# Kernel optimization log

Hardware: AMD Instinct MI355X
Metric: run time of the kernel (lower is better)

## Reference

```python
import jax, jax.numpy as jnp
import numpy as np
import math

B, T, D, H, FF = 2, 2048, 1024, 16, 4096
DH = D // H
EPS = 1e-5

def _ternary(key, out_f, in_f):
    # TFLELayer: ternary-quantized linear weight in {-1,0,1} (stored as f32 here)
    return jax.random.randint(key, (out_f, in_f), -1, 2).astype(jnp.float32)

def setup_inputs() -> dict:
    key = jax.random.key(0)
    ks = jax.random.split(key, 8)
    x = jax.random.normal(ks[0], (B, T, D), dtype=jnp.float32)
    mask = jnp.triu(jnp.ones((T, T), dtype=bool), k=1)  # True = masked (causal)
    return {
        "x": x,
        "mask": mask,
        "ln1_g": jnp.ones((D,), jnp.float32), "ln1_b": jnp.zeros((D,), jnp.float32),
        "ln2_g": jnp.ones((D,), jnp.float32), "ln2_b": jnp.zeros((D,), jnp.float32),
        "Wq": _ternary(ks[1], D, D), "Wk": _ternary(ks[2], D, D),
        "Wv": _ternary(ks[3], D, D), "Wo": _ternary(ks[4], D, D),
        "Wff1": _ternary(ks[5], FF, D), "Wff2": _ternary(ks[6], D, FF),
    }

def _ln(x, g, b):
    mu = jnp.mean(x, axis=-1, keepdims=True)
    var = jnp.var(x, axis=-1, keepdims=True)
    return (x - mu) * jax.lax.rsqrt(var + EPS) * g + b

def reference(x, mask, ln1_g, ln1_b, ln2_g, ln2_b, Wq, Wk, Wv, Wo, Wff1, Wff2):
    h = _ln(x, ln1_g, ln1_b)
    q = (h @ Wq.T).reshape(B, T, H, DH).transpose(0, 2, 1, 3)  # (B,H,T,DH)
    k = (h @ Wk.T).reshape(B, T, H, DH).transpose(0, 2, 1, 3)
    v = (h @ Wv.T).reshape(B, T, H, DH).transpose(0, 2, 1, 3)
    scale = 1.0 / math.sqrt(DH)
    attn = jnp.einsum('bhqd,bhkd->bhqk', q, k) * scale
    attn = jnp.where(mask[None, None], -jnp.inf, attn)
    attn = jax.nn.softmax(attn, axis=-1)
    out = jnp.einsum('bhqk,bhkd->bhqd', attn, v)
    out = out.transpose(0, 2, 1, 3).reshape(B, T, D) @ Wo.T
    x = x + out
    h = _ln(x, ln2_g, ln2_b)
    ff = jax.nn.gelu(h @ Wff1.T, approximate=False)
    ff = ff @ Wff2.T
    return x + ff
```

## Files before the change

kernel.cpp:

```cpp
#include <hip/hip_runtime.h>

typedef __bf16 bf16;
typedef bf16 bf16x8 __attribute__((ext_vector_type(8)));
typedef bf16 bf16x4 __attribute__((ext_vector_type(4)));
typedef float f32x4 __attribute__((ext_vector_type(4)));

static __device__ __forceinline__ void async16(const void* g, void* l) {
  __builtin_amdgcn_global_load_lds((__attribute__((address_space(1))) void*)g,
                                   (__attribute__((address_space(3))) void*)l,
                                   16, 0, 0);
}

template <int N>
static __device__ __forceinline__ float ror16(float x) {
  const int y =
      __builtin_amdgcn_update_dpp(0, __float_as_int(x), 0x120 | N, 0xf, 0xf, true);
  return __int_as_float(y);
}
static __device__ __forceinline__ float rowmax16(float x) {
  x = fmaxf(x, ror16<8>(x));
  x = fmaxf(x, ror16<4>(x));
  x = fmaxf(x, ror16<2>(x));
  x = fmaxf(x, ror16<1>(x));
  return x;
}
static __device__ __forceinline__ float rowsum16(float x) {
  x += ror16<8>(x);
  x += ror16<4>(x);
  x += ror16<2>(x);
  x += ror16<1>(x);
  return x;
}

__global__ __launch_bounds__(256) void cvt4(const float* __restrict__ a,
                                            const float* __restrict__ b,
                                            const float* __restrict__ c,
                                            const float* __restrict__ d,
                                            bf16* __restrict__ dst) {
  const size_t i = ((size_t)blockIdx.x * 256 + threadIdx.x) * 4;
  const size_t M1 = 1u << 20;
  const float* src = (i < M1) ? a : (i < 2 * M1) ? b : (i < 3 * M1) ? c : d;
  const size_t off = i & (M1 - 1);
  const float4 v = *(const float4*)(src + off);
  bf16x4 o = {(bf16)v.x, (bf16)v.y, (bf16)v.z, (bf16)v.w};
  *(bf16x4*)(dst + i) = o;
}

__global__ __launch_bounds__(256) void cvt2(const float* __restrict__ a,
                                            const float* __restrict__ b,
                                            bf16* __restrict__ dst) {
  const size_t i = ((size_t)blockIdx.x * 256 + threadIdx.x) * 4;
  const size_t M4 = 4u << 20;
  const float* src = (i < M4) ? a : b;
  const size_t off = (i < M4) ? i : i - M4;
  const float4 v = *(const float4*)(src + off);
  bf16x4 o = {(bf16)v.x, (bf16)v.y, (bf16)v.z, (bf16)v.w};
  *(bf16x4*)(dst + i) = o;
}

template <int EPI, bool SPLIT>
static __device__ __forceinline__ void gemm_body(
    const bf16* __restrict__ A, const bf16* __restrict__ A2,
    const bf16* __restrict__ B, void* __restrict__ Cv, void* __restrict__ C2,
    const float* __restrict__ R, float scale, int col0, int row0, int M, int N,
    int K) {
  __shared__ bf16 sA[128 * 32];
  __shared__ bf16 sB[128 * 32];
  const int tid = threadIdx.x;
  const int lane = tid & 63;
  const int wid = tid >> 6;
  const int wm = wid >> 1, wn = wid & 1;

  f32x4 acc[4][4];
  const f32x4 fzero = {0.f, 0.f, 0.f, 0.f};
#pragma unroll
  for (int i = 0; i < 4; ++i)
#pragma unroll
    for (int j = 0; j < 4; ++j) acc[i][j] = fzero;

  const int nk = K >> 5;
  const int total = SPLIT ? (nk << 1) : nk;
  const int r0 = tid >> 2, c0 = (tid & 3) << 3;
  const int r1 = (256 + tid) >> 2, c1 = ((256 + tid) & 3) << 3;
  bf16* lA0 = sA + (wid << 6) * 8;
  bf16* lA1 = sA + (256 + (wid << 6)) * 8;
  bf16* lB0 = sB + (wid << 6) * 8;
  bf16* lB1 = sB + (256 + (wid << 6)) * 8;

  for (int kt = 0; kt < total; ++kt) {
    const int kk = (kt < nk) ? kt : kt - nk;
    const bf16* Ap = (SPLIT && kt >= nk) ? A2 : A;
    const int k0 = kk << 5;
    async16(Ap + (size_t)(row0 + r0) * K + k0 + c0, lA0);
    async16(Ap + (size_t)(row0 + r1) * K + k0 + c1, lA1);
    async16(B + (size_t)(col0 + r0) * K + k0 + c0, lB0);
    async16(B + (size_t)(col0 + r1) * K + k0 + c1, lB1);
    __syncthreads();
    const int fr = lane & 15, fq = (lane >> 4) << 3;
    bf16x8 af[4], bfr[4];
#pragma unroll
    for (int i = 0; i < 4; ++i)
      af[i] = *(const bf16x8*)&sA[(wm * 64 + i * 16 + fr) * 32 + fq];
#pragma unroll
    for (int j = 0; j < 4; ++j)
      bfr[j] = *(const bf16x8*)&sB[(wn * 64 + j * 16 + fr) * 32 + fq];
#pragma unroll
    for (int i = 0; i < 4; ++i)
#pragma unroll
      for (int j = 0; j < 4; ++j)
        acc[i][j] = __builtin_amdgcn_mfma_f32_16x16x32_bf16(af[i], bfr[j],
                                                            acc[i][j], 0, 0, 0);
    __syncthreads();
  }

  const int fr = lane & 15, fq4 = (lane >> 4) << 2;
#pragma unroll
  for (int i = 0; i < 4; ++i) {
#pragma unroll
    for (int j = 0; j < 4; ++j) {
      const int rbase = row0 + wm * 64 + i * 16 + fq4;
      const int col = col0 + wn * 64 + j * 16 + fr;
      if constexpr (EPI == 5) {
        const int b = rbase >> 11, t = rbase & 2047;
        const int hh = col >> 6, d = col & 63;
        bf16x4 o4 = {(bf16)acc[i][j][0], (bf16)acc[i][j][1],
                     (bf16)acc[i][j][2], (bf16)acc[i][j][3]};
        *(bf16x4*)&((bf16*)Cv)[(((size_t)(b * 16 + hh)) * 64 + d) * 2048 + t] =
            o4;
      } else {
#pragma unroll
        for (int r = 0; r < 4; ++r) {
          const size_t idx = (size_t)(rbase + r) * N + col;
          const float val = acc[i][j][r];
          if constexpr (EPI == 0) {
            ((float*)Cv)[idx] = val;
          } else if constexpr (EPI == 2) {
            ((float*)Cv)[idx] = val + R[idx];
          } else if constexpr (EPI == 3) {
            ((bf16*)Cv)[idx] =
                (bf16)(0.5f * val * (1.0f + erff(val * 0.7071067811865476f)));
          } else {
            const float vs = val * scale;
            const bf16 hi = (bf16)vs;
            ((bf16*)Cv)[idx] = hi;
            ((bf16*)C2)[idx] = (bf16)(vs - (float)hi);
          }
        }
      }
    }
  }
}

template <int EPI, bool SPLIT>
__global__ __launch_bounds__(256) void gemm_bt(
    const bf16* __restrict__ A, const bf16* __restrict__ A2,
    const bf16* __restrict__ B, void* __restrict__ Cv,
    const float* __restrict__ R, int M, int N, int K) {
  gemm_body<EPI, SPLIT>(A, A2, B, Cv, nullptr, R, 1.0f, blockIdx.x * 128,
                        blockIdx.y * 128, M, N, K);
}

static __device__ __forceinline__ void gemm_split_merged(
    const bf16* __restrict__ A, const bf16* __restrict__ A2,
    const bf16* __restrict__ B, bf16* __restrict__ Chi, bf16* __restrict__ Clo,
    float scale, int col0, int row0) {
  constexpr int K = 1024, N = 1024;
  __shared__ bf16 sAh[128 * 32];
  __shared__ bf16 sAl[128 * 32];
  __shared__ bf16 sB[128 * 32];
  const int tid = threadIdx.x;
  const int lane = tid & 63;
  const int wid = tid >> 6;
  const int wm = wid >> 1, wn = wid & 1;

  f32x4 acc[4][4];
  const f32x4 fzero = {0.f, 0.f, 0.f, 0.f};
#pragma unroll
  for (int i = 0; i < 4; ++i)
#pragma unroll
    for (int j = 0; j < 4; ++j) acc[i][j] = fzero;

  const int r0 = tid >> 2, c0 = (tid & 3) << 3;
  const int r1 = (256 + tid) >> 2, c1 = ((256 + tid) & 3) << 3;
  bf16* lAh0 = sAh + (wid << 6) * 8;
  bf16* lAh1 = sAh + (256 + (wid << 6)) * 8;
  bf16* lAl0 = sAl + (wid << 6) * 8;
  bf16* lAl1 = sAl + (256 + (wid << 6)) * 8;
  bf16* lB0 = sB + (wid << 6) * 8;
  bf16* lB1 = sB + (256 + (wid << 6)) * 8;

  for (int kt = 0; kt < 32; ++kt) {
    const int k0 = kt << 5;
    async16(A + (size_t)(row0 + r0) * K + k0 + c0, lAh0);
    async16(A + (size_t)(row0 + r1) * K + k0 + c1, lAh1);
    async16(A2 + (size_t)(row0 + r0) * K + k0 + c0, lAl0);
    async16(A2 + (size_t)(row0 + r1) * K + k0 + c1, lAl1);
    async16(B + (size_t)(col0 + r0) * K + k0 + c0, lB0);
    async16(B + (size_t)(col0 + r1) * K + k0 + c1, lB1);
    __syncthreads();
    const int fr = lane & 15, fq = (lane >> 4) << 3;
    bf16x8 ah[4], al[4], bfr[4];
#pragma unroll
    for (int i = 0; i < 4; ++i) {
      ah[i] = *(const bf16x8*)&sAh[(wm * 64 + i * 16 + fr) * 32 + fq];
      al[i] = *(const bf16x8*)&sAl[(wm * 64 + i * 16 + fr) * 32 + fq];
    }
#pragma unroll
    for (int j = 0; j < 4; ++j)
      bfr[j] = *(const bf16x8*)&sB[(wn * 64 + j * 16 + fr) * 32 + fq];
#pragma unroll
    for (int i = 0; i < 4; ++i)
#pragma unroll
      for (int j = 0; j < 4; ++j) {
        acc[i][j] = __builtin_amdgcn_mfma_f32_16x16x32_bf16(ah[i], bfr[j],
                                                            acc[i][j], 0, 0, 0);
        acc[i][j] = __builtin_amdgcn_mfma_f32_16x16x32_bf16(al[i], bfr[j],
                                                            acc[i][j], 0, 0, 0);
      }
    __syncthreads();
  }

  const int fr = lane & 15, fq4 = (lane >> 4) << 2;
#pragma unroll
  for (int i = 0; i < 4; ++i)
#pragma unroll
    for (int j = 0; j < 4; ++j) {
      const int rbase = row0 + wm * 64 + i * 16 + fq4;
      const int col = col0 + wn * 64 + j * 16 + fr;
#pragma unroll
      for (int r = 0; r < 4; ++r) {
        const size_t idx = (size_t)(rbase + r) * N + col;
        const float vs = acc[i][j][r] * scale;
        const bf16 hi = (bf16)vs;
        Chi[idx] = hi;
        Clo[idx] = (bf16)(vs - (float)hi);
      }
    }
}

__global__ __launch_bounds__(256) void gemm_qkv(
    const bf16* __restrict__ A, const bf16* __restrict__ A2,
    const bf16* __restrict__ Bq, const bf16* __restrict__ Bk,
    const bf16* __restrict__ Bv, bf16* qh, bf16* ql, bf16* kh, bf16* kl,
    bf16* vt) {
  const int which = blockIdx.x >> 3;
  const int col0 = (blockIdx.x & 7) * 128, row0 = blockIdx.y * 128;
  if (which == 2) {
    gemm_body<5, false>(A, nullptr, Bv, (void*)vt, nullptr, nullptr, 1.0f,
                        col0, row0, 4096, 1024, 1024);
  } else {
    gemm_split_merged(A, A2, which ? Bk : Bq, which ? kh : qh, which ? kl : ql,
                      which ? 1.0f : 0.125f, col0, row0);
  }
}

template <int EPI>
__global__ __launch_bounds__(256) void gemm_bt64(
    const bf16* __restrict__ A, const bf16* __restrict__ B,
    void* __restrict__ Cv, const float* __restrict__ R, int M, int N, int K) {
  __shared__ bf16 sA[128 * 32];
  __shared__ bf16 sB[64 * 32];
  const int col0 = blockIdx.x * 64, row0 = blockIdx.y * 128;
  const int tid = threadIdx.x;
  const int lane = tid & 63;
  const int wid = tid >> 6;
  const int wm = wid >> 1, wn = wid & 1;

  f32x4 acc[4][2];
  const f32x4 fzero = {0.f, 0.f, 0.f, 0.f};
#pragma unroll
  for (int i = 0; i < 4; ++i)
#pragma unroll
    for (int j = 0; j < 2; ++j) acc[i][j] = fzero;

  const int nk = K >> 5;
  const int r0 = tid >> 2, c0 = (tid & 3) << 3;
  const int r1 = (256 + tid) >> 2, c1 = ((256 + tid) & 3) << 3;
  bf16* lA0 = sA + (wid << 6) * 8;
  bf16* lA1 = sA + (256 + (wid << 6)) * 8;
  bf16* lB0 = sB + (wid << 6) * 8;

  for (int kt = 0; kt < nk; ++kt) {
    const int k0 = kt << 5;
    async16(A + (size_t)(row0 + r0) * K + k0 + c0, lA0);
    async16(A + (size_t)(row0 + r1) * K + k0 + c1, lA1);
    async16(B + (size_t)(col0 + r0) * K + k0 + c0, lB0);
    __syncthreads();
    const int fr = lane & 15, fq = (lane >> 4) << 3;
    bf16x8 af[4], bfr[2];
#pragma unroll
    for (int i = 0; i < 4; ++i)
      af[i] = *(const bf16x8*)&sA[(wm * 64 + i * 16 + fr) * 32 + fq];
#pragma unroll
    for (int j = 0; j < 2; ++j)
      bfr[j] = *(const bf16x8*)&sB[(wn * 32 + j * 16 + fr) * 32 + fq];
#pragma unroll
    for (int i = 0; i < 4; ++i)
#pragma unroll
      for (int j = 0; j < 2; ++j)
        acc[i][j] = __builtin_amdgcn_mfma_f32_16x16x32_bf16(af[i], bfr[j],
                                                            acc[i][j], 0, 0, 0);
    __syncthreads();
  }

  const int fr = lane & 15, fq4 = (lane >> 4) << 2;
#pragma unroll
  for (int i = 0; i < 4; ++i) {
#pragma unroll
    for (int j = 0; j < 2; ++j) {
      const int rbase = row0 + wm * 64 + i * 16 + fq4;
      const int col = col0 + wn * 32 + j * 16 + fr;
#pragma unroll
      for (int r = 0; r < 4; ++r) {
        const size_t idx = (size_t)(rbase + r) * N + col;
        const float val = acc[i][j][r];
        if constexpr (EPI == 2) {
          ((float*)Cv)[idx] = val + R[idx];
        } else {
          ((float*)Cv)[idx] = val;
        }
      }
    }
  }
}

template <bool SPLIT>
__global__ __launch_bounds__(256) void ln_kernel(
    const float* __restrict__ x, const float* __restrict__ g,
    const float* __restrict__ b, bf16* __restrict__ hi, bf16* __restrict__ lo) {
  const int row = blockIdx.x;
  const int tid = threadIdx.x;
  const float* xr = x + (size_t)row * 1024;
  float v[4];
  float s1 = 0.f, s2 = 0.f;
#pragma unroll
  for (int j = 0; j < 4; ++j) {
    v[j] = xr[j * 256 + tid];
    s1 += v[j];
    s2 += v[j] * v[j];
  }
#pragma unroll
  for (int off = 1; off < 64; off <<= 1) {
    s1 += __shfl_xor(s1, off);
    s2 += __shfl_xor(s2, off);
  }
  __shared__ float ws1[4], ws2[4];
  const int wid = tid >> 6;
  if ((tid & 63) == 0) {
    ws1[wid] = s1;
    ws2[wid] = s2;
  }
  __syncthreads();
  s1 = ws1[0] + ws1[1] + ws1[2] + ws1[3];
  s2 = ws2[0] + ws2[1] + ws2[2] + ws2[3];
  const float mu = s1 * (1.f / 1024.f);
  const float var = s2 * (1.f / 1024.f) - mu * mu;
  const float rstd = 1.0f / sqrtf(var + 1e-5f);
#pragma unroll
  for (int j = 0; j < 4; ++j) {
    const int cc = j * 256 + tid;
    const float y = (v[j] - mu) * rstd * g[cc] + b[cc];
    const bf16 yh = (bf16)y;
    hi[(size_t)row * 1024 + cc] = yh;
    if constexpr (SPLIT) lo[(size_t)row * 1024 + cc] = (bf16)(y - (float)yh);
  }
}

__global__ __launch_bounds__(256) void attn_kernel(
    const bf16* __restrict__ qh_g, const bf16* __restrict__ ql_g,
    const bf16* __restrict__ kh_g, const bf16* __restrict__ kl_g,
    const bf16* __restrict__ vt_g, bf16* __restrict__ out) {
  __shared__ bf16 lds[18688];
  bf16* Kh = lds;
  bf16* Kl = lds + 4608;
  bf16* Vt = lds + 9216;
  bf16* Ps = lds + 13824;

  const int bid = blockIdx.x;
  const int qt = 31 - (bid >> 5);
  const int h = bid & 15;
  const int b = (bid >> 4) & 1;
  const int t0 = qt << 6;
  const int tid = threadIdx.x;
  const int w = tid >> 6;
  const int lane = tid & 63;
  const int c = lane & 15;
  const int quad = lane >> 4;

  const int r0 = tid >> 3, c0 = (tid & 7) << 3;
  const int r1 = (tid + 256) >> 3, c1 = ((tid + 256) & 7) << 3;

  const size_t qrow =
      ((size_t)(b * 2048 + t0 + w * 16 + c)) * 1024 + h * 64 + quad * 8;
  bf16x8 aqh[2], aql[2];
  aqh[0] = *(const bf16x8*)&qh_g[qrow];
  aqh[1] = *(const bf16x8*)&qh_g[qrow + 32];
  aql[0] = *(const bf16x8*)&ql_g[qrow];
  aql[1] = *(const bf16x8*)&ql_g[qrow + 32];

  f32x4 o[4];
  const f32x4 fzero = {0.f, 0.f, 0.f, 0.f};
#pragma unroll
  for (int j = 0; j < 4; ++j) o[j] = fzero;
  float m_i[4] = {-3e38f, -3e38f, -3e38f, -3e38f};
  float l_i[4] = {0.f, 0.f, 0.f, 0.f};

  const size_t vtb = ((size_t)(b * 16 + h)) * 64 * 2048;
  const size_t kband = ((size_t)(b * 2048)) * 1024 + h * 64;

  bf16x8 gk[6];
  {
    gk[0] = *(const bf16x8*)&kh_g[kband + (size_t)r0 * 1024 + c0];
    gk[1] = *(const bf16x8*)&kh_g[kband + (size_t)r1 * 1024 + c1];
    gk[2] = *(const bf16x8*)&kl_g[kband + (size_t)r0 * 1024 + c0];
    gk[3] = *(const bf16x8*)&kl_g[kband + (size_t)r1 * 1024 + c1];
    gk[4] = *(const bf16x8*)&vt_g[vtb + (size_t)r0 * 2048 + c0];
    gk[5] = *(const bf16x8*)&vt_g[vtb + (size_t)r1 * 2048 + c1];
  }

  for (int kt = 0; kt <= qt; ++kt) {
    __syncthreads();
    *(bf16x8*)&Kh[r0 * 72 + c0] = gk[0];
    *(bf16x8*)&Kh[r1 * 72 + c1] = gk[1];
    *(bf16x8*)&Kl[r0 * 72 + c0] = gk[2];
    *(bf16x8*)&Kl[r1 * 72 + c1] = gk[3];
    *(bf16x8*)&Vt[r0 * 72 + c0] = gk[4];
    *(bf16x8*)&Vt[r1 * 72 + c1] = gk[5];
    __syncthreads();

    if (kt < qt) {
      const int kb1 = (kt + 1) << 6;
      const size_t kbase = kband + (size_t)kb1 * 1024;
      gk[0] = *(const bf16x8*)&kh_g[kbase + (size_t)r0 * 1024 + c0];
      gk[1] = *(const bf16x8*)&kh_g[kbase + (size_t)r1 * 1024 + c1];
      gk[2] = *(const bf16x8*)&kl_g[kbase + (size_t)r0 * 1024 + c0];
      gk[3] = *(const bf16x8*)&kl_g[kbase + (size_t)r1 * 1024 + c1];
      gk[4] = *(const bf16x8*)&vt_g[vtb + (size_t)r0 * 2048 + kb1 + c0];
      gk[5] = *(const bf16x8*)&vt_g[vtb + (size_t)r1 * 2048 + kb1 + c1];
    }

    bf16x8 bkh[4][2], bkl[4][2];
#pragma unroll
    for (int j = 0; j < 4; ++j)
#pragma unroll
      for (int s = 0; s < 2; ++s) {
        bkh[j][s] = *(const bf16x8*)&Kh[(j * 16 + c) * 72 + s * 32 + quad * 8];
        bkl[j][s] = *(const bf16x8*)&Kl[(j * 16 + c) * 72 + s * 32 + quad * 8];
      }

    f32x4 s4[4];
#pragma unroll
    for (int j = 0; j < 4; ++j) s4[j] = fzero;
#pragma unroll
    for (int j = 0; j < 4; ++j)
#pragma unroll
      for (int s = 0; s < 2; ++s) {
        s4[j] = __builtin_amdgcn_mfma_f32_16x16x32_bf16(aqh[s], bkh[j][s], s4[j], 0, 0, 0);
        s4[j] = __builtin_amdgcn_mfma_f32_16x16x32_bf16(aqh[s], bkl[j][s], s4[j], 0, 0, 0);
        s4[j] = __builtin_amdgcn_mfma_f32_16x16x32_bf16(aql[s], bkh[j][s], s4[j], 0, 0, 0);
      }

    if (kt == qt) {
#pragma unroll
      for (int j = 0; j < 4; ++j)
#pragma unroll
        for (int r = 0; r < 4; ++r)
          if (j * 16 + c > w * 16 + quad * 4 + r) s4[j][r] = -3e38f;
    }

    float al[4], p[4][4];
#pragma unroll
    for (int r = 0; r < 4; ++r) {
      float mt = fmaxf(fmaxf(s4[0][r], s4[1][r]), fmaxf(s4[2][r], s4[3][r]));
      mt = rowmax16(mt);
      const float mn = fmaxf(m_i[r], mt);
      al[r] = __expf(m_i[r] - mn);
      float ps = 0.f;
#pragma unroll
      for (int j = 0; j < 4; ++j) {
        p[r][j] = __expf(s4[j][r] - mn);
        ps += p[r][j];
      }
      ps = rowsum16(ps);
      l_i[r] = l_i[r] * al[r] + ps;
      m_i[r] = mn;
#pragma unroll
      for (int j = 0; j < 4; ++j) o[j][r] *= al[r];
    }

    bf16* Pw = Ps + w * 16 * 76;
#pragma unroll
    for (int r = 0; r < 4; ++r)
#pragma unroll
      for (int j = 0; j < 4; ++j)
        Pw[(quad * 4 + r) * 76 + j * 16 + c] = (bf16)p[r][j];

    bf16x8 ap[2], bv[4][2];
#pragma unroll
    for (int s = 0; s < 2; ++s)
      ap[s] = *(const bf16x8*)&Pw[c * 76 + s * 32 + quad * 8];
#pragma unroll
    for (int j = 0; j < 4; ++j)
#pragma unroll
      for (int s = 0; s < 2; ++s)
        bv[j][s] = *(const bf16x8*)&Vt[(j * 16 + c) * 72 + s * 32 + quad * 8];
#pragma unroll
    for (int j = 0; j < 4; ++j)
#pragma unroll
      for (int s = 0; s < 2; ++s)
        o[j] = __builtin_amdgcn_mfma_f32_16x16x32_bf16(ap[s], bv[j][s], o[j], 0, 0, 0);
  }

#pragma unroll
  for (int r = 0; r < 4; ++r) {
    const float inv = 1.0f / l_i[r];
#pragma unroll
    for (int j = 0; j < 4; ++j) {
      const size_t oi =
          ((size_t)(b * 2048 + t0 + w * 16 + quad * 4 + r)) * 1024 + h * 64 +
          j * 16 + c;
      out[oi] = (bf16)(o[j][r] * inv);
    }
  }
}

extern "C" void kernel_launch(void* const* d_in, const int* in_sizes, int n_in,
                              void* d_out, int out_size, void* d_ws,
                              size_t ws_size, hipStream_t stream) {
  const float* x = (const float*)d_in[0];
  const float* g1 = (const float*)d_in[2];
  const float* b1 = (const float*)d_in[3];
  const float* g2 = (const float*)d_in[4];
  const float* b2 = (const float*)d_in[5];
  const float* Wq = (const float*)d_in[6];
  const float* Wk = (const float*)d_in[7];
  const float* Wv = (const float*)d_in[8];
  const float* Wo = (const float*)d_in[9];
  const float* Wf1 = (const float*)d_in[10];
  const float* Wf2 = (const float*)d_in[11];
  char* ws = (char*)d_ws;
  const size_t MB = 1024 * 1024;
  const size_t M1 = 1u << 20;
  bf16* Wq_b = (bf16*)ws;
  bf16* Wk_b = Wq_b + 1 * M1;
  bf16* Wv_b = Wq_b + 2 * M1;
  bf16* Wo_b = Wq_b + 3 * M1;
  bf16* h_hi = (bf16*)(ws + 8 * MB);
  bf16* h_lo = (bf16*)(ws + 16 * MB);
  bf16* Wf1_b = h_hi;
  bf16* Wf2_b = h_lo;
  bf16* qh = (bf16*)(ws + 24 * MB);
  bf16* ql = (bf16*)(ws + 32 * MB);
  bf16* kh = (bf16*)(ws + 40 * MB);
  bf16* kl = (bf16*)(ws + 48 * MB);
  bf16* vt = (bf16*)(ws + 56 * MB);
  bf16* attnout = (bf16*)(ws + 64 * MB);
  float* x1 = (float*)qh;
  bf16* h2 = (bf16*)(ws + 72 * MB);
  bf16* ff = kh;
  float* outp = (float*)d_out;

  cvt4<<<4096, 256, 0, stream>>>(Wq, Wk, Wv, Wo, Wq_b);
  ln_kernel<true><<<4096, 256, 0, stream>>>(x, g1, b1, h_hi, h_lo);
  gemm_qkv<<<dim3(24, 32), 256, 0, stream>>>(h_hi, h_lo, Wq_b, Wk_b, Wv_b, qh,
                                             ql, kh, kl, vt);
  cvt2<<<8192, 256, 0, stream>>>(Wf1, Wf2, Wf1_b);
  attn_kernel<<<1024, 256, 0, stream>>>(qh, ql, kh, kl, vt, attnout);
  gemm_bt64<2><<<dim3(16, 32), 256, 0, stream>>>(attnout, Wo_b, (void*)x1, x,
                                                 4096, 1024, 1024);
  ln_kernel<false><<<4096, 256, 0, stream>>>(x1, g2, b2, h2, nullptr);
  gemm_bt<3, false><<<dim3(32, 32), 256, 0, stream>>>(
      h2, nullptr, Wf1_b, (void*)ff, nullptr, 4096, 4096, 1024);
  gemm_bt64<2><<<dim3(16, 32), 256, 0, stream>>>(ff, Wf2_b, (void*)outp, x1,
                                                 4096, 1024, 4096);
}
```

Baseline: 465.6 us.

## Double attention query tile per block and share LDS across QKV GEMM paths

The attention kernel now handles 128 query rows per block: each wave processes two 16-row sub-tiles against the same K/V tile loaded into LDS. This halves the grid and the repeated K/V global loads per query row. The block order is also changed to interleave long and short causal tiles. Separately, the QKV GEMM paths now take one shared LDS buffer instead of separate static arrays, which lowers that kernel's LDS footprint. The larger attention tile raises register pressure and leaves fewer blocks to balance the causal work.

```diff
diff --git a/kernel.cpp b/kernel.cpp
--- a/kernel.cpp
+++ b/kernel.cpp
@@ -61,11 +61,11 @@
 template <int EPI, bool SPLIT>
 static __device__ __forceinline__ void gemm_body(
     const bf16* __restrict__ A, const bf16* __restrict__ A2,
-    const bf16* __restrict__ B, void* __restrict__ Cv, void* __restrict__ C2,
-    const float* __restrict__ R, float scale, int col0, int row0, int M, int N,
+    const bf16* __restrict__ B, void* __restrict__ Cv,
+    const float* __restrict__ R, bf16* smem, int col0, int row0, int M, int N,
     int K) {
-  __shared__ bf16 sA[128 * 32];
-  __shared__ bf16 sB[128 * 32];
+  bf16* sA = smem;
+  bf16* sB = smem + 4096;
   const int tid = threadIdx.x;
   const int lane = tid & 63;
   const int wid = tid >> 6;
@@ -136,14 +136,9 @@
             ((float*)Cv)[idx] = val;
           } else if constexpr (EPI == 2) {
             ((float*)Cv)[idx] = val + R[idx];
-          } else if constexpr (EPI == 3) {
+          } else {
             ((bf16*)Cv)[idx] =
                 (bf16)(0.5f * val * (1.0f + erff(val * 0.7071067811865476f)));
-          } else {
-            const float vs = val * scale;
-            const bf16 hi = (bf16)vs;
-            ((bf16*)Cv)[idx] = hi;
-            ((bf16*)C2)[idx] = (bf16)(vs - (float)hi);
           }
         }
       }
@@ -156,18 +151,19 @@
     const bf16* __restrict__ A, const bf16* __restrict__ A2,
     const bf16* __restrict__ B, void* __restrict__ Cv,
     const float* __restrict__ R, int M, int N, int K) {
-  gemm_body<EPI, SPLIT>(A, A2, B, Cv, nullptr, R, 1.0f, blockIdx.x * 128,
+  __shared__ bf16 smem[8192];
+  gemm_body<EPI, SPLIT>(A, A2, B, Cv, R, smem, blockIdx.x * 128,
                         blockIdx.y * 128, M, N, K);
 }
 
 static __device__ __forceinline__ void gemm_split_merged(
     const bf16* __restrict__ A, const bf16* __restrict__ A2,
     const bf16* __restrict__ B, bf16* __restrict__ Chi, bf16* __restrict__ Clo,
-    float scale, int col0, int row0) {
+    bf16* smem, float scale, int col0, int row0) {
   constexpr int K = 1024, N = 1024;
-  __shared__ bf16 sAh[128 * 32];
-  __shared__ bf16 sAl[128 * 32];
-  __shared__ bf16 sB[128 * 32];
+  bf16* sAh = smem;
+  bf16* sAl = smem + 4096;
+  bf16* sB = smem + 8192;
   const int tid = threadIdx.x;
   const int lane = tid & 63;
   const int wid = tid >> 6;
@@ -243,14 +239,15 @@
     const bf16* __restrict__ Bq, const bf16* __restrict__ Bk,
     const bf16* __restrict__ Bv, bf16* qh, bf16* ql, bf16* kh, bf16* kl,
     bf16* vt) {
+  __shared__ bf16 smem[12288];
   const int which = blockIdx.x >> 3;
   const int col0 = (blockIdx.x & 7) * 128, row0 = blockIdx.y * 128;
   if (which == 2) {
-    gemm_body<5, false>(A, nullptr, Bv, (void*)vt, nullptr, nullptr, 1.0f,
-                        col0, row0, 4096, 1024, 1024);
+    gemm_body<5, false>(A, nullptr, Bv, (void*)vt, nullptr, smem, col0, row0,
+                        4096, 1024, 1024);
   } else {
     gemm_split_merged(A, A2, which ? Bk : Bq, which ? kh : qh, which ? kl : ql,
-                      which ? 1.0f : 0.125f, col0, row0);
+                      smem, which ? 1.0f : 0.125f, col0, row0);
   }
 }
 
@@ -377,10 +374,11 @@
   bf16* Ps = lds + 13824;
 
   const int bid = blockIdx.x;
-  const int qt = 31 - (bid >> 5);
+  const int g = bid >> 5;
+  const int qt = (g < 8) ? (15 - g) : (g - 8);
   const int h = bid & 15;
   const int b = (bid >> 4) & 1;
-  const int t0 = qt << 6;
+  const int t0 = qt << 7;
   const int tid = threadIdx.x;
   const int w = tid >> 6;
   const int lane = tid & 63;
@@ -390,23 +388,36 @@
   const int r0 = tid >> 3, c0 = (tid & 7) << 3;
   const int r1 = (tid + 256) >> 3, c1 = ((tid + 256) & 7) << 3;
 
-  const size_t qrow =
-      ((size_t)(b * 2048 + t0 + w * 16 + c)) * 1024 + h * 64 + quad * 8;
-  bf16x8 aqh[2], aql[2];
-  aqh[0] = *(const bf16x8*)&qh_g[qrow];
-  aqh[1] = *(const bf16x8*)&qh_g[qrow + 32];
-  aql[0] = *(const bf16x8*)&ql_g[qrow];
-  aql[1] = *(const bf16x8*)&ql_g[qrow + 32];
-
-  f32x4 o[4];
+  bf16x8 aqh[2][2], aql[2][2];
+#pragma unroll
+  for (int u = 0; u < 2; ++u) {
+    const size_t qrow =
+        ((size_t)(b * 2048 + t0 + w * 32 + u * 16 + c)) * 1024 + h * 64 +
+        quad * 8;
+    aqh[u][0] = *(const bf16x8*)&qh_g[qrow];
+    aqh[u][1] = *(const bf16x8*)&qh_g[qrow + 32];
+    aql[u][0] = *(const bf16x8*)&ql_g[qrow];
+    aql[u][1] = *(const bf16x8*)&ql_g[qrow + 32];
+  }
+
+  f32x4 o[2][4];
   const f32x4 fzero = {0.f, 0.f, 0.f, 0.f};
 #pragma unroll
-  for (int j = 0; j < 4; ++j) o[j] = fzero;
-  float m_i[4] = {-3e38f, -3e38f, -3e38f, -3e38f};
-  float l_i[4] = {0.f, 0.f, 0.f, 0.f};
+  for (int u = 0; u < 2; ++u)
+#pragma unroll
+    for (int j = 0; j < 4; ++j) o[u][j] = fzero;
+  float m_i[2][4], l_i[2][4];
+#pragma unroll
+  for (int u = 0; u < 2; ++u)
+#pragma unroll
+    for (int r = 0; r < 4; ++r) {
+      m_i[u][r] = -3e38f;
+      l_i[u][r] = 0.f;
+    }
 
   const size_t vtb = ((size_t)(b * 16 + h)) * 64 * 2048;
   const size_t kband = ((size_t)(b * 2048)) * 1024 + h * 64;
+  const int nt = 2 * qt + 2;
 
   bf16x8 gk[6];
   {
@@ -418,7 +429,8 @@
     gk[5] = *(const bf16x8*)&vt_g[vtb + (size_t)r1 * 2048 + c1];
   }
 
-  for (int kt = 0; kt <= qt; ++kt) {
+  for (int kt = 0; kt < nt; ++kt) {
+    const int kb = kt << 6;
     __syncthreads();
     *(bf16x8*)&Kh[r0 * 72 + c0] = gk[0];
     *(bf16x8*)&Kh[r1 * 72 + c1] = gk[1];
@@ -428,7 +440,7 @@
     *(bf16x8*)&Vt[r1 * 72 + c1] = gk[5];
     __syncthreads();
 
-    if (kt < qt) {
+    if (kt < nt - 1) {
       const int kb1 = (kt + 1) << 6;
       const size_t kbase = kband + (size_t)kb1 * 1024;
       gk[0] = *(const bf16x8*)&kh_g[kbase + (size_t)r0 * 1024 + c0];
@@ -439,89 +451,95 @@
       gk[5] = *(const bf16x8*)&vt_g[vtb + (size_t)r1 * 2048 + kb1 + c1];
     }
 
-    bf16x8 bkh[4][2], bkl[4][2];
+    bf16x8 bkh[4][2], bkl[4][2], bv[4][2];
 #pragma unroll
     for (int j = 0; j < 4; ++j)
 #pragma unroll
       for (int s = 0; s < 2; ++s) {
         bkh[j][s] = *(const bf16x8*)&Kh[(j * 16 + c) * 72 + s * 32 + quad * 8];
         bkl[j][s] = *(const bf16x8*)&Kl[(j * 16 + c) * 72 + s * 32 + quad * 8];
-      }
-
-    f32x4 s4[4];
-#pragma unroll
-    for (int j = 0; j < 4; ++j) s4[j] = fzero;
-#pragma unroll
-    for (int j = 0; j < 4; ++j)
-#pragma unroll
-      for (int s = 0; s < 2; ++s) {
-        s4[j] = __builtin_amdgcn_mfma_f32_16x16x32_bf16(aqh[s], bkh[j][s], s4[j], 0, 0, 0);
-        s4[j] = __builtin_amdgcn_mfma_f32_16x16x32_bf16(aqh[s], bkl[j][s], s4[j], 0, 0, 0);
-        s4[j] = __builtin_amdgcn_mfma_f32_16x16x32_bf16(aql[s], bkh[j][s], s4[j], 0, 0, 0);
-      }
-
-    if (kt == qt) {
+        bv[j][s] = *(const bf16x8*)&Vt[(j * 16 + c) * 72 + s * 32 + quad * 8];
+      }
+
+    bf16* Pw = Ps + w * 16 * 76;
+#pragma unroll
+    for (int u = 0; u < 2; ++u) {
+      f32x4 s4[4];
+#pragma unroll
+      for (int j = 0; j < 4; ++j) s4[j] = fzero;
 #pragma unroll
       for (int j = 0; j < 4; ++j)
 #pragma unroll
-        for (int r = 0; r < 4; ++r)
-          if (j * 16 + c > w * 16 + quad * 4 + r) s4[j][r] = -3e38f;
-    }
-
-    float al[4], p[4][4];
+        for (int s = 0; s < 2; ++s) {
+          s4[j] = __builtin_amdgcn_mfma_f32_16x16x32_bf16(aqh[u][s], bkh[j][s],
+                                                          s4[j], 0, 0, 0);
+          s4[j] = __builtin_amdgcn_mfma_f32_16x16x32_bf16(aqh[u][s], bkl[j][s],
+                                                          s4[j], 0, 0, 0);
+          s4[j] = __builtin_amdgcn_mfma_f32_16x16x32_bf16(aql[u][s], bkh[j][s],
+                                                          s4[j], 0, 0, 0);
+        }
+
+      if (kt >= 2 * qt) {
+        const int qrow0 = t0 + w * 32 + u * 16 + quad * 4;
+#pragma unroll
+        for (int j = 0; j < 4; ++j)
+#pragma unroll
+          for (int r = 0; r < 4; ++r)
+            if (kb + j * 16 + c > qrow0 + r) s4[j][r] = -3e38f;
+      }
+
+      float al[4], p[4][4];
+#pragma unroll
+      for (int r = 0; r < 4; ++r) {
+        float mt = fmaxf(fmaxf(s4[0][r], s4[1][r]), fmaxf(s4[2][r], s4[3][r]));
+        mt = rowmax16(mt);
+        const float mn = fmaxf(m_i[u][r], mt);
+        al[r] = __expf(m_i[u][r] - mn);
+        float ps = 0.f;
+#pragma unroll
+        for (int j = 0; j < 4; ++j) {
+          p[r][j] = __expf(s4[j][r] - mn);
+          ps += p[r][j];
+        }
+        ps = rowsum16(ps);
+        l_i[u][r] = l_i[u][r] * al[r] + ps;
+        m_i[u][r] = mn;
+#pragma unroll
+        for (int j = 0; j < 4; ++j) o[u][j][r] *= al[r];
+      }
+
+#pragma unroll
+      for (int r = 0; r < 4; ++r)
+#pragma unroll
+        for (int j = 0; j < 4; ++j)
+          Pw[(quad * 4 + r) * 76 + j * 16 + c] = (bf16)p[r][j];
+
+      bf16x8 ap[2];
+#pragma unroll
+      for (int s = 0; s < 2; ++s)
+        ap[s] = *(const bf16x8*)&Pw[c * 76 + s * 32 + quad * 8];
+#pragma unroll
+      for (int j = 0; j < 4; ++j)
+#pragma unroll
+        for (int s = 0; s < 2; ++s)
+          o[u][j] = __builtin_amdgcn_mfma_f32_16x16x32_bf16(ap[s], bv[j][s],
+                                                            o[u][j], 0, 0, 0);
+    }
+  }
+
+#pragma unroll
+  for (int u = 0; u < 2; ++u)
 #pragma unroll
     for (int r = 0; r < 4; ++r) {
-      float mt = fmaxf(fmaxf(s4[0][r], s4[1][r]), fmaxf(s4[2][r], s4[3][r]));
-      mt = rowmax16(mt);
-      const float mn = fmaxf(m_i[r], mt);
-      al[r] = __expf(m_i[r] - mn);
-      float ps = 0.f;
+      const float inv = 1.0f / l_i[u][r];
 #pragma unroll
       for (int j = 0; j < 4; ++j) {
-        p[r][j] = __expf(s4[j][r] - mn);
-        ps += p[r][j];
-      }
-      ps = rowsum16(ps);
-      l_i[r] = l_i[r] * al[r] + ps;
-      m_i[r] = mn;
-#pragma unroll
-      for (int j = 0; j < 4; ++j) o[j][r] *= al[r];
-    }
-
-    bf16* Pw = Ps + w * 16 * 76;
-#pragma unroll
-    for (int r = 0; r < 4; ++r)
-#pragma unroll
-      for (int j = 0; j < 4; ++j)
-        Pw[(quad * 4 + r) * 76 + j * 16 + c] = (bf16)p[r][j];
-
-    bf16x8 ap[2], bv[4][2];
-#pragma unroll
-    for (int s = 0; s < 2; ++s)
-      ap[s] = *(const bf16x8*)&Pw[c * 76 + s * 32 + quad * 8];
-#pragma unroll
-    for (int j = 0; j < 4; ++j)
-#pragma unroll
-      for (int s = 0; s < 2; ++s)
-        bv[j][s] = *(const bf16x8*)&Vt[(j * 16 + c) * 72 + s * 32 + quad * 8];
-#pragma unroll
-    for (int j = 0; j < 4; ++j)
-#pragma unroll
-      for (int s = 0; s < 2; ++s)
-        o[j] = __builtin_amdgcn_mfma_f32_16x16x32_bf16(ap[s], bv[j][s], o[j], 0, 0, 0);
-  }
-
-#pragma unroll
-  for (int r = 0; r < 4; ++r) {
-    const float inv = 1.0f / l_i[r];
-#pragma unroll
-    for (int j = 0; j < 4; ++j) {
-      const size_t oi =
-          ((size_t)(b * 2048 + t0 + w * 16 + quad * 4 + r)) * 1024 + h * 64 +
-          j * 16 + c;
-      out[oi] = (bf16)(o[j][r] * inv);
-    }
-  }
+        const size_t oi =
+            ((size_t)(b * 2048 + t0 + w * 32 + u * 16 + quad * 4 + r)) * 1024 +
+            h * 64 + j * 16 + c;
+        out[oi] = (bf16)(o[u][j][r] * inv);
+      }
+    }
 }
 
 extern "C" void kernel_launch(void* const* d_in, const int* in_sizes, int n_in,
@@ -565,7 +583,7 @@
   gemm_qkv<<<dim3(24, 32), 256, 0, stream>>>(h_hi, h_lo, Wq_b, Wk_b, Wv_b, qh,
                                              ql, kh, kl, vt);
   cvt2<<<8192, 256, 0, stream>>>(Wf1, Wf2, Wf1_b);
-  attn_kernel<<<1024, 256, 0, stream>>>(qh, ql, kh, kl, vt, attnout);
+  attn_kernel<<<512, 256, 0, stream>>>(qh, ql, kh, kl, vt, attnout);
   gemm_bt64<2><<<dim3(16, 32), 256, 0, stream>>>(attnout, Wo_b, (void*)x1, x,
                                                  4096, 1024, 1024);
   ln_kernel<false><<<4096, 256, 0, stream>>>(x1, g2, b2, h2, nullptr);
```

Measured after the change: 488.3 us. 4.9% more time.
